# Optimization experiments

Measured on AMD Instinct MI355X. Metric: run time of the kernel, lower is better.

Reference implementation:

```python
import jax, jax.numpy as jnp
import numpy as np

B, D, N, H = 2, 512, 2048, 8
DK = D // H
EPS = 1e-5


def conv1x1(x, w, b):
    # kernel-size-1 Conv1d == channel-mixing GEMM: (o,i) x (b,i,n) -> (b,o,n)
    return jnp.einsum('oi,bin->bon', w, x) + b[None, :, None]


def setup_inputs() -> dict:
    key = jax.random.key(0)
    ks = jax.random.split(key, 20)
    s = 0.02
    return {
        'init_query': jax.random.normal(ks[0], (B, D, N), jnp.float32),
        'key_t': jax.random.normal(ks[1], (B, D, N), jnp.float32),
        'value': jax.random.normal(ks[2], (B, D, N), jnp.float32),
        'mask': jax.random.randint(ks[3], (B, 1, N, N), 0, 2, jnp.int32),
        'Wq': jax.random.normal(ks[4], (D, D), jnp.float32) * s,
        'bq': jax.random.normal(ks[5], (D,), jnp.float32) * s,
        'Wk': jax.random.normal(ks[6], (D, D), jnp.float32) * s,
        'bk': jax.random.normal(ks[7], (D,), jnp.float32) * s,
        'Wv': jax.random.normal(ks[8], (D, D), jnp.float32) * s,
        'bv': jax.random.normal(ks[9], (D,), jnp.float32) * s,
        'Wm': jax.random.normal(ks[10], (D, D), jnp.float32) * s,
        'bm': jax.random.normal(ks[11], (D,), jnp.float32) * s,
        'W1': jax.random.normal(ks[12], (2 * D, 2 * D), jnp.float32) * s,
        'b1': jax.random.normal(ks[13], (2 * D,), jnp.float32) * s,
        'gamma': jnp.ones((2 * D,), jnp.float32),
        'beta': jnp.zeros((2 * D,), jnp.float32),
        'rmean': jax.random.normal(ks[14], (2 * D,), jnp.float32) * s,
        'rvar': jnp.abs(jax.random.normal(ks[15], (2 * D,), jnp.float32)) * 0.1 + 0.5,
        'W2': jax.random.normal(ks[16], (D, 2 * D), jnp.float32) * s,
        'b2': jnp.zeros((D,), jnp.float32),  # nn.init.constant_(bias, 0.0)
    }


def reference(init_query, key_t, value, mask, Wq, bq, Wk, bk, Wv, bv, Wm, bm,
              W1, b1, gamma, beta, rmean, rvar, W2, b2):
    # projections, split channels into (d_k, n_heads) exactly like torch .view
    q = conv1x1(init_query, Wq, bq).reshape(B, DK, H, N)
    k = conv1x1(key_t, Wk, bk).reshape(B, DK, H, N)
    v = conv1x1(value, Wv, bv).reshape(B, DK, H, N)
    scores = jnp.einsum('bdhn,bdhm->bhnm', q, k) / jnp.sqrt(jnp.float32(DK))
    scores = jnp.where(mask == 0, jnp.float32(-1e9), scores)
    attn = jax.nn.softmax(scores, axis=-1)
    x = jnp.einsum('bhnm,bdhm->bdhn', attn, v).reshape(B, D, N)
    x = conv1x1(x, Wm, bm)
    x = jnp.concatenate([x, init_query], axis=1)  # (B, 2D, N)
    h = conv1x1(x, W1, b1)
    # BatchNorm1d (inference mode with running stats) + ReLU
    h = (h - rmean[None, :, None]) * (gamma / jnp.sqrt(rvar + EPS))[None, :, None] + beta[None, :, None]
    h = jax.nn.relu(h)
    return conv1x1(h, W2, b2)
```

## Files before the change

### kernel.cpp

```cpp
#include <hip/hip_runtime.h>

typedef unsigned short u16;
typedef unsigned int u32;
typedef unsigned long long u64;
typedef long long i64;
typedef __bf16 bf16x8 __attribute__((ext_vector_type(8)));
typedef u16 u16x8 __attribute__((ext_vector_type(8)));
typedef float f32x4 __attribute__((ext_vector_type(4)));
typedef float f32x16 __attribute__((ext_vector_type(16)));

#define DEV __device__ __forceinline__

constexpr int BB = 2, DD = 512, NN = 2048, HH = 8, DKc = 64, D2 = 1024;

constexpr float QSC = 0.125f * 1.44269504088896340736f;

constexpr i64 MB = 1048576;
constexpr i64 OFF_CAT = 0;
constexpr i64 OFF_XKT = 8 * MB;
constexpr i64 OFF_XVT = 12 * MB;
constexpr i64 OFF_QH  = 16 * MB;
constexpr i64 OFF_KH  = 20 * MB;
constexpr i64 OFF_VT  = 24 * MB;
constexpr i64 OFF_HT  = 28 * MB;
constexpr i64 OFF_OP  = 36 * MB;
constexpr i64 OFF_LP  = 68 * MB;
constexpr i64 OFF_WQP = 69 * MB;
constexpr i64 OFF_WKP = 69 * MB + 524288;
constexpr i64 OFF_WVP = 69 * MB + 1048576;
constexpr i64 OFF_WMT = 69 * MB + 1572864;
constexpr i64 OFF_W1A = 71 * MB;
constexpr i64 OFF_W1C = 72 * MB;
constexpr i64 OFF_W2B = 74 * MB;
constexpr i64 OFF_BQP = 75 * MB;
constexpr i64 OFF_BKP = 75 * MB + 2048;
constexpr i64 OFF_BVP = 75 * MB + 4096;
constexpr i64 OFF_BNA = 75 * MB + 8192;
constexpr i64 OFF_BNC = 75 * MB + 12288;
constexpr i64 OFF_MSK = 76 * MB;

DEV u16 f2bf(float f) {
  u32 u = __float_as_uint(f);
  u = u + 0x7FFFu + ((u >> 16) & 1u);
  return (u16)(u >> 16);
}

DEV float bf2f(u16 u) { return __uint_as_float(((u32)u) << 16); }
DEV float bf2f32(u32 u) { return __uint_as_float(u << 16); }

DEV u32 packbf(float lo, float hi) {
  return __builtin_amdgcn_perm(__float_as_uint(hi), __float_as_uint(lo), 0x07060302u);
}

DEV float fexp2(float x) {
#if __has_builtin(__builtin_amdgcn_exp2f)
  return __builtin_amdgcn_exp2f(x);
#else
  return exp2f(x);
#endif
}

DEV bf16x8 ldfrag(const u16* p) {
  bf16x8 v;
  __builtin_memcpy(&v, __builtin_assume_aligned(p, 16), 16);
  return v;
}

DEV bf16x8 ldfrag2(const u16* p0, const u16* p1) {
  bf16x8 v;
  __builtin_memcpy(&v, __builtin_assume_aligned(p0, 8), 8);
  __builtin_memcpy((char*)&v + 8, __builtin_assume_aligned(p1, 8), 8);
  return v;
}

DEV bf16x8 ones8() {
  u16x8 u = {0x3F80, 0x3F80, 0x3F80, 0x3F80, 0x3F80, 0x3F80, 0x3F80, 0x3F80};
  bf16x8 v;
  __builtin_memcpy(&v, &u, 16);
  return v;
}

DEV void gload16(const void* g, void* lds) {
  __builtin_amdgcn_global_load_lds((__attribute__((address_space(1))) void*)g,
                                   (__attribute__((address_space(3))) void*)lds, 16, 0, 0);
}

DEV f32x4 mfma16(bf16x8 a, bf16x8 b, f32x4 c) {
  return __builtin_amdgcn_mfma_f32_16x16x32_bf16(a, b, c, 0, 0, 0);
}

DEV f32x16 mfma32(bf16x8 a, bf16x8 b, f32x16 c) {
  return __builtin_amdgcn_mfma_f32_32x32x16_bf16(a, b, c, 0, 0, 0);
}

__global__ __launch_bounds__(256) void prep_all(
    const float* __restrict__ Wq, const float* __restrict__ Wk, const float* __restrict__ Wv,
    const float* __restrict__ Wm, const float* __restrict__ W1, const float* __restrict__ W2,
    const float* __restrict__ bq, const float* __restrict__ bk, const float* __restrict__ bv,
    const float* __restrict__ bm, const float* __restrict__ b1, const float* __restrict__ gamma_,
    const float* __restrict__ beta_, const float* __restrict__ rmean,
    const float* __restrict__ rvar, const int* __restrict__ mask,
    const float* __restrict__ iq, const float* __restrict__ kt, const float* __restrict__ vv,
    u16* __restrict__ wqp, u16* __restrict__ wkp, u16* __restrict__ wvp, u16* __restrict__ wmt,
    u16* __restrict__ w1a, u16* __restrict__ w1c, u16* __restrict__ w2b,
    float* __restrict__ bqp, float* __restrict__ bkp, float* __restrict__ bvp,
    float* __restrict__ bna, float* __restrict__ bnc, u32* __restrict__ mw,
    u16* __restrict__ cat, u16* __restrict__ xkt, u16* __restrict__ xvt) {
  __shared__ float tile[32][33];
  const int blk = blockIdx.x, t = threadIdx.x;
  if (blk < 768) {
    const int which = blk >> 8, lb = blk & 255;
    const float* W = which == 0 ? Wq : (which == 1 ? Wk : Wv);
    u16* dst = which == 0 ? wqp : (which == 1 ? wkp : wvp);
    for (int e = lb * 256 + t; e < 262144; e += 65536) {
      int op = e >> 9, i = e & 511;
      int dk = op & 63, h = op >> 6;
      dst[e] = f2bf(W[(dk * 8 + h) * 512 + i]);
    }
  } else if (blk < 1024) {
    const int lb = blk - 768;
    for (int e = lb * 256 + t; e < 262144; e += 65536) {
      int cp = e >> 9, o = e & 511;
      int dk = cp & 63, h = cp >> 6;
      wmt[e] = f2bf(Wm[o * 512 + dk * 8 + h]);
    }
  } else if (blk < 1280) {
    const int lb = blk - 1024;
    for (int e = lb * 256 + t; e < 524288; e += 65536) {
      int row = e >> 9, o = e & 511;
      w1a[e] = f2bf(W1[(i64)row * 1024 + o]);
    }
  } else if (blk < 1536) {
    const int lb = blk - 1280;
    for (int e = lb * 256 + t; e < 524288; e += 65536) {
      int row = e >> 9, j = e & 511;
      w1c[(i64)row * 1024 + 512 + j] = f2bf(W1[(i64)row * 1024 + 512 + j]);
    }
  } else if (blk < 1792) {
    const int lb = blk - 1536;
    for (int e = lb * 256 + t; e < 524288; e += 65536) w2b[e] = f2bf(W2[e]);
  } else if (blk < 1808) {
    __shared__ float sm[4][64];
    const int base = (blk - 1792) * 64;
    const int el = t & 63, oq = t >> 6;
    const float* wrow = W1 + (i64)(base + el) * 1024 + oq * 128;
    const float* bmq = bm + oq * 128;
    float s = 0.f;
#pragma unroll 8
    for (int j = 0; j < 128; j += 4) {
      float4 x = *(const float4*)(wrow + j);
      float4 y = *(const float4*)(bmq + j);
      s += x.x * y.x + x.y * y.y + x.z * y.z + x.w * y.w;
    }
    sm[oq][el] = s;
    __syncthreads();
    if (t < 64) {
      int e = base + t;
      float a = gamma_[e] * rsqrtf(rvar[e] + 1e-5f);
      bna[e] = a;
      bnc[e] = (b1[e] - rmean[e]) * a + beta_[e] + a * (sm[0][t] + sm[1][t] + sm[2][t] + sm[3][t]);
    }
  } else if (blk == 1808) {
    for (int e = t; e < 512; e += 256) {
      int src = (e & 63) * 8 + (e >> 6);
      bqp[e] = bq[src]; bkp[e] = bk[src]; bvp[e] = bv[src];
    }
  } else if (blk < 2833) {
    const int tid = (blk - 1809) * 256 + t;
    const i64 base = (i64)tid * 32;
    const int4* mp = (const int4*)(mask + base);
    u32 word = 0;
#pragma unroll
    for (int j = 0; j < 8; ++j) {
      int4 x = mp[j];
      u32 nib = (x.x != 0 ? 1u : 0u) | (x.y != 0 ? 2u : 0u) | (x.z != 0 ? 4u : 0u) |
                (x.w != 0 ? 8u : 0u);
      word |= nib << (j * 4);
    }
    mw[tid] = word;
  } else {
    const int idx = blk - 2833;
    const int bx = idx & 63, by = (idx >> 6) & 15, bz = idx >> 10;
    const int tensor = bz >> 1, b = bz & 1;
    const float* src = (tensor == 0 ? iq : (tensor == 1 ? kt : vv)) + (i64)b * DD * NN;
    u16* dst; i64 ldd; int coff;
    if (tensor == 0)      { dst = cat + (i64)b * NN * D2; ldd = D2; coff = DD; }
    else if (tensor == 1) { dst = xkt + (i64)b * NN * DD; ldd = DD; coff = 0; }
    else                  { dst = xvt + (i64)b * NN * DD; ldd = DD; coff = 0; }
    const int x0 = bx * 32, y0 = by * 32;
    const int col = t & 31, rg = t >> 5;
#pragma unroll
    for (int i = 0; i < 4; ++i) {
      int row = rg + i * 8;
      tile[row][col] = src[(i64)(y0 + row) * NN + x0 + col];
    }
    __syncthreads();
    const int dp = t & 15, rbase = t >> 4;
    u32* dst32 = (u32*)dst;
    const i64 ldw = ldd >> 1;
    const int cw = (coff + y0) >> 1;
#pragma unroll
    for (int i = 0; i < 2; ++i) {
      int rr = rbase + i * 16;
      dst32[(i64)(x0 + rr) * ldw + cw + dp] = packbf(tile[2 * dp][rr], tile[2 * dp + 1][rr]);
    }
  }
}

template <int AM, int AN>
DEV void gemm_core(const u16* __restrict__ A, i64 lda, const u16* __restrict__ Bp, i64 ldb,
                   int K, u16* As, u16* Bs, f32x4 (&acc)[AM][AN]) {
  constexpr int BM = AM * 32, BN = AN * 32;
  const int t = threadIdx.x, w = t >> 6, l = t & 63, quad = l >> 4, l15 = l & 15;
  const int wm = (w >> 1) * AM * 16, wn = (w & 1) * AN * 16;
  for (int kk = 0; kk < K; kk += 64) {
    __syncthreads();
#pragma unroll
    for (int j = 0; j < BM / 32; ++j) {
      int ch = j * 256 + w * 64 + l, r = ch >> 3, c = ch & 7;
      gload16(A + (i64)r * lda + kk + ((c ^ (r & 7)) << 3), As + (j * 256 + w * 64) * 8);
    }
#pragma unroll
    for (int j = 0; j < BN / 32; ++j) {
      int ch = j * 256 + w * 64 + l, r = ch >> 3, c = ch & 7;
      gload16(Bp + (i64)r * ldb + kk + ((c ^ (r & 7)) << 3), Bs + (j * 256 + w * 64) * 8);
    }
    __syncthreads();
#pragma unroll
    for (int kc = 0; kc < 2; ++kc) {
      const int sw = ((kc * 4 + quad) ^ (l15 & 7)) << 3;
      bf16x8 af[AM], bfr[AN];
#pragma unroll
      for (int i = 0; i < AM; ++i) af[i] = ldfrag(&As[(wm + i * 16 + l15) * 64 + sw]);
#pragma unroll
      for (int j = 0; j < AN; ++j) bfr[j] = ldfrag(&Bs[(wn + j * 16 + l15) * 64 + sw]);
#pragma unroll
      for (int i = 0; i < AM; ++i)
#pragma unroll
        for (int j = 0; j < AN; ++j) acc[i][j] = mfma16(af[i], bfr[j], acc[i][j]);
    }
  }
}

__global__ __launch_bounds__(256) void qkv_gemm(const u16* __restrict__ cat,
                                                const u16* __restrict__ xkt,
                                                const u16* __restrict__ xvt,
                                                const u16* __restrict__ wqp,
                                                const u16* __restrict__ wkp,
                                                const u16* __restrict__ wvp,
                                                const u16* __restrict__ w1a,
                                                const u16* __restrict__ wmt,
                                                const float* __restrict__ bqp,
                                                const float* __restrict__ bkp,
                                                const float* __restrict__ bvp,
                                                u16* __restrict__ qh, u16* __restrict__ kh,
                                                u16* __restrict__ vt, u16* __restrict__ w1c) {
  __shared__ __align__(16) u16 As[128 * 64];
  __shared__ __align__(16) u16 Bs[128 * 64];
  const int flat = blockIdx.x;
  const int t = threadIdx.x, w = t >> 6, l = t & 63, quad = l >> 4, l15 = l & 15;
  const int wm = (w >> 1) * 64, wn = (w & 1) * 64;
  int op, b = 0, mx, ny;
  if (flat < 256) {
    op = flat >> 7;
    b = (flat >> 6) & 1;
    const int r = flat & 63;
    mx = r >> 2; ny = r & 3;
  } else if (flat < 384) {
    op = 2;
    const int r = flat - 256;
    b = r >> 6;
    const int rr = r & 63;
    mx = rr >> 4; ny = rr & 15;
  } else {
    op = 3;
    const int r = flat - 384;
    mx = r >> 2; ny = r & 3;
  }
  const u16 *A, *Bp;
  i64 lda, ldb;
  if (op < 2) {
    A = (op == 0 ? cat + DD : xkt);
    lda = (op == 0 ? D2 : DD);
    A += (i64)b * NN * lda + (i64)mx * 128 * lda;
    Bp = (op == 0 ? wqp : wkp) + (i64)ny * 128 * DD;
    ldb = DD;
  } else if (op == 2) {
    A = wvp + (i64)mx * 128 * DD; lda = DD;
    Bp = xvt + (i64)b * NN * DD + (i64)ny * 128 * DD; ldb = DD;
  } else {
    A = w1a + (i64)mx * 128 * DD; lda = DD;
    Bp = wmt + (i64)ny * 128 * DD; ldb = DD;
  }
  f32x4 acc[4][4] = {};
  gemm_core<4, 4>(A, lda, Bp, ldb, DD, As, Bs, acc);

  const int rowBase = mx * 128 + wm + quad * 4;
  const int colBase = ny * 128 + wn + l15;
  if (op < 2) {
    const float* bias = (op == 0 ? bqp : bkp);
    const float sc = (op == 0 ? QSC : 1.f);
    u16* dst = (op == 0 ? qh : kh) + (i64)b * HH * NN * DKc;
#pragma unroll
    for (int j = 0; j < 4; ++j) {
      const int col = colBase + j * 16;
      const float cA = bias[col];
#pragma unroll
      for (int i = 0; i < 4; ++i)
#pragma unroll
        for (int r = 0; r < 4; ++r) {
          const int row = rowBase + i * 16 + r;
          dst[(i64)(col >> 6) * (NN * 64) + (i64)row * 64 + (col & 63)] =
              f2bf((acc[i][j][r] + cA) * sc);
        }
    }
  } else if (op == 2) {
    u16* dst = vt + (i64)b * HH * DKc * NN;
#pragma unroll
    for (int j = 0; j < 4; ++j) {
      const int col = colBase + j * 16;
#pragma unroll
      for (int i = 0; i < 4; ++i)
#pragma unroll
        for (int r = 0; r < 4; ++r) {
          const int row = rowBase + i * 16 + r;
          dst[(i64)row * NN + col] = f2bf(acc[i][j][r] + bvp[row]);
        }
    }
  } else {
#pragma unroll
    for (int j = 0; j < 4; ++j) {
      const int col = colBase + j * 16;
#pragma unroll
      for (int i = 0; i < 4; ++i)
#pragma unroll
        for (int r = 0; r < 4; ++r) {
          const int row = rowBase + i * 16 + r;
          w1c[(i64)row * D2 + col] = f2bf(acc[i][j][r]);
        }
    }
  }
}

struct GArgs {
  const u16* A; i64 lda, sAb;
  const u16* B; i64 ldb, sBb;
  void* C; i64 ldc, sCb;
  const float* p1; const float* p2;
  int K;
};

template <int MODE, int AM, int AN, int SWZ>
__global__ __launch_bounds__(256) void gemm_bt(GArgs g) {
  __shared__ __align__(16) u16 As[AM * 32 * 64];
  __shared__ __align__(16) u16 Bs[AN * 32 * 64];
  const int t = threadIdx.x, w = t >> 6, l = t & 63, quad = l >> 4, l15 = l & 15;
  const int wm = (w >> 1) * AM * 16, wn = (w & 1) * AN * 16;
  int bx = blockIdx.x, by = blockIdx.y, bz = blockIdx.z;
  if (SWZ == 1) {
    const int i = bx + (by << 3) + (bz << 8);
    const int slot = i & 7, jj = i >> 3;
    by = slot + ((jj & 3) << 3);
    const int j2 = jj >> 2;
    bx = j2 & 7;
    bz = j2 >> 3;
  }
  const u16* A = g.A + (i64)bz * g.sAb + (i64)bx * (AM * 32) * g.lda;
  const u16* Bp = g.B + (i64)bz * g.sBb + (i64)by * (AN * 32) * g.ldb;
  f32x4 acc[AM][AN] = {};
  gemm_core<AM, AN>(A, g.lda, Bp, g.ldb, g.K, As, Bs, acc);

  const int rowBase = bx * (AM * 32) + wm + quad * 4;
  const int colBase = by * (AN * 32) + wn + l15;
#pragma unroll
  for (int j = 0; j < AN; ++j) {
    const int col = colBase + j * 16;
    float cA = 0.f, cB = 0.f;
    if (MODE == 3) { cA = g.p1[col]; cB = g.p2[col]; }
#pragma unroll
    for (int i = 0; i < AM; ++i) {
#pragma unroll
      for (int r = 0; r < 4; ++r) {
        const int row = rowBase + i * 16 + r;
        float v = acc[i][j][r];
        if (MODE == 3) {
          float x = v * cA + cB;
          ((u16*)g.C + (i64)bz * g.sCb)[(i64)row * g.ldc + col] = f2bf(x > 0.f ? x : 0.f);
        } else {
          ((float*)g.C + (i64)bz * g.sCb)[(i64)row * g.ldc + col] = v + g.p1[row];
        }
      }
    }
  }
}

__global__ __launch_bounds__(512) void flash_attn(const u16* __restrict__ Qh,
                                                  const u16* __restrict__ Kh,
                                                  const u16* __restrict__ Vt,
                                                  const u64* __restrict__ MW64,
                                                  u16* __restrict__ Opart,
                                                  float* __restrict__ Lp) {
  __shared__ __align__(16) u16 Ks0[64 * 64];
  __shared__ __align__(16) u16 Ks1[64 * 64];
  __shared__ __align__(16) u16 Vs0[64 * 64];
  __shared__ __align__(16) u16 Vs1[64 * 64];
  const int t = threadIdx.x, w = t >> 6, l = t & 63, l31 = l & 31, lh = l >> 5;
  const int flat = blockIdx.x;
  const int h = flat & 7;
  const int j = flat >> 3;
  const int nt = j & 7, zz = j >> 3;
  const int sp = zz & 3, b = zz >> 2;
  const int n = nt * 256 + w * 32 + l31;
  const u16* Qb = Qh + ((i64)(b * HH + h) * NN + nt * 256 + w * 32) * 64;
  const u16* Kb = Kh + (i64)(b * HH + h) * NN * 64;
  const u16* Vb = Vt + (i64)(b * HH + h) * 64 * NN;
  const u64* mwp = MW64 + (i64)(b * NN + n) * 32;
  const bf16x8 ONE = ones8();
  bf16x8 qf[4];
#pragma unroll
  for (int kc = 0; kc < 4; ++kc)
    __builtin_memcpy(&qf[kc], Qb + (i64)l31 * 64 + kc * 16 + lh * 8, 16);

  f32x16 oacc0 = {}, oacc1 = {}, lacc = {};
  const int mt0 = sp * 8;

  auto stage = [&](u16* Kd, u16* Vd, int mt) {
    const int r = t >> 3, c = t & 7;
    gload16(Kb + (i64)(mt * 64 + r) * 64 + ((c ^ (r & 7)) << 3), Kd + t * 8);
    gload16(Vb + (i64)r * NN + mt * 64 + ((c ^ (r & 7)) << 3), Vd + t * 8);
  };
  auto compute = [&](const u16* Kc, const u16* Vc, int mt) {
    f32x16 s0 = {}, s1 = {};
#pragma unroll
    for (int kc = 0; kc < 4; ++kc) {
      const int sw = l31 & 7;
      bf16x8 k0 = ldfrag(&Kc[l31 * 64 + (((kc * 2 + lh) ^ sw) << 3)]);
      bf16x8 k1 = ldfrag(&Kc[(32 + l31) * 64 + (((kc * 2 + lh) ^ sw) << 3)]);
      s0 = mfma32(k0, qf[kc], s0);
      s1 = mfma32(k1, qf[kc], s1);
    }
    const u64 mrow = mwp[mt];
    u32 pw[16];
#pragma unroll
    for (int k = 0; k < 8; ++k) {
      const int kvb = ((2 * k) & 3) + 8 * ((2 * k) >> 2) + 4 * lh;
      u64 sh = mrow >> kvb;
      u32 mA = (((u32)sh & 1u) | (((u32)sh & 2u) << 15)) * 0xFFFFu;
      u32 shh = (u32)(sh >> 32);
      u32 mB = ((shh & 1u) | ((shh & 2u) << 15)) * 0xFFFFu;
      pw[k] = packbf(fexp2(s0[2 * k]), fexp2(s0[2 * k + 1])) & mA;
      pw[8 + k] = packbf(fexp2(s1[2 * k]), fexp2(s1[2 * k + 1])) & mB;
    }
    bf16x8 pf[4];
#pragma unroll
    for (int c = 0; c < 4; ++c) __builtin_memcpy(&pf[c], &pw[c * 4], 16);
#pragma unroll
    for (int c = 0; c < 4; ++c) lacc = mfma32(ONE, pf[c], lacc);
#pragma unroll
    for (int c = 0; c < 4; ++c) {
      const int sw0 = l31 & 7;
      const u16* r0 = &Vc[l31 * 64];
      const u16* r1 = &Vc[(32 + l31) * 64];
      bf16x8 v0 = ldfrag2(r0 + (((2 * c) ^ sw0) << 3) + lh * 4,
                          r0 + (((2 * c + 1) ^ sw0) << 3) + lh * 4);
      bf16x8 v1 = ldfrag2(r1 + (((2 * c) ^ sw0) << 3) + lh * 4,
                          r1 + (((2 * c + 1) ^ sw0) << 3) + lh * 4);
      oacc0 = mfma32(v0, pf[c], oacc0);
      oacc1 = mfma32(v1, pf[c], oacc1);
    }
  };

  stage(Ks0, Vs0, mt0);
#pragma unroll
  for (int i = 0; i < 8; i += 2) {
    __syncthreads();
    stage(Ks1, Vs1, mt0 + i + 1);
    compute(Ks0, Vs0, mt0 + i);
    __syncthreads();
    if (i + 2 < 8) stage(Ks0, Vs0, mt0 + i + 2);
    compute(Ks1, Vs1, mt0 + i + 1);
  }
  u16* OpT = Opart + ((i64)((sp * BB + b) * HH + h) * 64) * NN;
#pragma unroll
  for (int r = 0; r < 16; ++r) {
    const int d0 = (r & 3) + 8 * (r >> 2) + 4 * lh;
    OpT[(i64)d0 * NN + n] = f2bf(oacc0[r]);
    OpT[(i64)(d0 + 32) * NN + n] = f2bf(oacc1[r]);
  }
  if (lh == 0) Lp[((i64)(sp * BB + b) * HH + h) * NN + n] = lacc[0];
}

__global__ __launch_bounds__(256) void combine(const u16* __restrict__ Opart,
                                               const float* __restrict__ Lp,
                                               u16* __restrict__ cat) {
  __shared__ float lt[128 * 65];
  const int t = threadIdx.x;
  const int nt = blockIdx.x, bh = blockIdx.y;
  const int b = bh >> 3, h = bh & 7;
  const int n0 = nt * 128;
  const i64 sstride = (i64)BB * HH * 64 * NN;
  const u16* Ob = Opart + ((i64)(b * HH + h) * 64) * NN;
#pragma unroll
  for (int i = 0; i < 16; ++i) {
    const int idx = i * 256 + t;
    const int d = idx >> 6, np = idx & 63;
    float sa = 0.f, sb = 0.f;
#pragma unroll
    for (int s = 0; s < 4; ++s) {
      u32 v;
      __builtin_memcpy(&v, Ob + s * sstride + (i64)d * NN + n0 + 2 * np, 4);
      sa += bf2f32(v & 0xFFFFu);
      sb += bf2f32(v >> 16);
    }
    lt[(2 * np) * 65 + d] = sa;
    lt[(2 * np + 1) * 65 + d] = sb;
  }
  __syncthreads();
  u32* catw = (u32*)cat;
#pragma unroll
  for (int i = 0; i < 16; ++i) {
    const int idx = i * 256 + t;
    const int nn = idx >> 5, dp = idx & 31;
    float lsum = 0.f;
#pragma unroll
    for (int s = 0; s < 4; ++s) lsum += Lp[((i64)(s * BB + b) * HH + h) * NN + n0 + nn];
    const float rl = __builtin_amdgcn_rcpf(lsum);
    u32 pv = packbf(lt[nn * 65 + 2 * dp] * rl, lt[nn * 65 + 2 * dp + 1] * rl);
    catw[((i64)b * NN + n0 + nn) * (D2 / 2) + h * 32 + dp] = pv;
  }
}

extern "C" void kernel_launch(void* const* d_in, const int* in_sizes, int n_in,
                              void* d_out, int out_size, void* d_ws, size_t ws_size,
                              hipStream_t stream) {
  (void)in_sizes; (void)n_in; (void)out_size; (void)ws_size;
  const float* iq    = (const float*)d_in[0];
  const float* kt    = (const float*)d_in[1];
  const float* vv    = (const float*)d_in[2];
  const int*   mask  = (const int*)d_in[3];
  const float* Wq    = (const float*)d_in[4];
  const float* bq    = (const float*)d_in[5];
  const float* Wk    = (const float*)d_in[6];
  const float* bk    = (const float*)d_in[7];
  const float* Wv    = (const float*)d_in[8];
  const float* bv    = (const float*)d_in[9];
  const float* Wm    = (const float*)d_in[10];
  const float* bm    = (const float*)d_in[11];
  const float* W1    = (const float*)d_in[12];
  const float* b1    = (const float*)d_in[13];
  const float* gamma_= (const float*)d_in[14];
  const float* beta_ = (const float*)d_in[15];
  const float* rmean = (const float*)d_in[16];
  const float* rvar  = (const float*)d_in[17];
  const float* W2    = (const float*)d_in[18];
  const float* b2    = (const float*)d_in[19];

  char* ws = (char*)d_ws;
  u16* cat = (u16*)(ws + OFF_CAT);
  u16* xkt = (u16*)(ws + OFF_XKT);
  u16* xvt = (u16*)(ws + OFF_XVT);
  u16* qh  = (u16*)(ws + OFF_QH);
  u16* kh  = (u16*)(ws + OFF_KH);
  u16* vt  = (u16*)(ws + OFF_VT);
  u16* ht  = (u16*)(ws + OFF_HT);
  u16* opart = (u16*)(ws + OFF_OP);
  float* lp  = (float*)(ws + OFF_LP);
  u16* wqp = (u16*)(ws + OFF_WQP);
  u16* wkp = (u16*)(ws + OFF_WKP);
  u16* wvp = (u16*)(ws + OFF_WVP);
  u16* wmt = (u16*)(ws + OFF_WMT);
  u16* w1a = (u16*)(ws + OFF_W1A);
  u16* w1c = (u16*)(ws + OFF_W1C);
  u16* w2b = (u16*)(ws + OFF_W2B);
  float* bqp = (float*)(ws + OFF_BQP);
  float* bkp = (float*)(ws + OFF_BKP);
  float* bvp = (float*)(ws + OFF_BVP);
  float* bna = (float*)(ws + OFF_BNA);
  float* bnc = (float*)(ws + OFF_BNC);
  u32* mw = (u32*)(ws + OFF_MSK);

  prep_all<<<8977, 256, 0, stream>>>(Wq, Wk, Wv, Wm, W1, W2, bq, bk, bv, bm, b1, gamma_, beta_,
                                     rmean, rvar, mask, iq, kt, vv, wqp, wkp, wvp, wmt, w1a, w1c,
                                     w2b, bqp, bkp, bvp, bna, bnc, mw, cat, xkt, xvt);
  qkv_gemm<<<416, 256, 0, stream>>>(cat, xkt, xvt, wqp, wkp, wvp, w1a, wmt,
                                    bqp, bkp, bvp, qh, kh, vt, w1c);
  flash_attn<<<512, 512, 0, stream>>>(qh, kh, vt, (const u64*)mw, opart, lp);
  combine<<<dim3(16, 16), 256, 0, stream>>>(opart, lp, cat);
  GArgs wa{cat, D2, 0, w1c, D2, 0, ht, D2, 0, bna, bnc, D2};
  gemm_bt<3, 4, 2, 0><<<dim3(32, 16, 1), 256, 0, stream>>>(wa);
  GArgs w2a{w2b, D2, 0, ht, D2, (i64)NN * D2, d_out, NN, (i64)DD * NN, b2, nullptr, D2};
  gemm_bt<4, 2, 2, 1><<<dim3(8, 32, 2), 256, 0, stream>>>(w2a);
}
```

Before: 216.5 us.

## Double-buffer shared-memory tiles in GEMM core to overlap loads with MFMA

Turns the GEMM main loop into a two-stage pipeline. The next K-slice is loaded asynchronously into a second LDS buffer while the current slice feeds MFMA, with one barrier per iteration instead of two. Shared-memory footprint doubles in both qkv_gemm and gemm_bt, which may lower occupancy. Because of the full vmcnt(0) wait at the end of each iteration, the overlap is limited to the MFMA work within that iteration.

```diff
diff --git a/kernel.cpp b/kernel.cpp
--- a/kernel.cpp
+++ b/kernel.cpp
@@ -213,32 +213,43 @@
   constexpr int BM = AM * 32, BN = AN * 32;
   const int t = threadIdx.x, w = t >> 6, l = t & 63, quad = l >> 4, l15 = l & 15;
   const int wm = (w >> 1) * AM * 16, wn = (w & 1) * AN * 16;
-  for (int kk = 0; kk < K; kk += 64) {
-    __syncthreads();
+  auto stage = [&](int kk, int buf) {
+    u16* Ad = As + buf * (BM * 64);
+    u16* Bd = Bs + buf * (BN * 64);
 #pragma unroll
     for (int j = 0; j < BM / 32; ++j) {
       int ch = j * 256 + w * 64 + l, r = ch >> 3, c = ch & 7;
-      gload16(A + (i64)r * lda + kk + ((c ^ (r & 7)) << 3), As + (j * 256 + w * 64) * 8);
+      gload16(A + (i64)r * lda + kk + ((c ^ (r & 7)) << 3), Ad + (j * 256 + w * 64) * 8);
     }
 #pragma unroll
     for (int j = 0; j < BN / 32; ++j) {
       int ch = j * 256 + w * 64 + l, r = ch >> 3, c = ch & 7;
-      gload16(Bp + (i64)r * ldb + kk + ((c ^ (r & 7)) << 3), Bs + (j * 256 + w * 64) * 8);
-    }
-    __syncthreads();
+      gload16(Bp + (i64)r * ldb + kk + ((c ^ (r & 7)) << 3), Bd + (j * 256 + w * 64) * 8);
+    }
+  };
+  const int nst = K >> 6;
+  stage(0, 0);
+  asm volatile("s_waitcnt vmcnt(0)" ::: "memory");
+  __builtin_amdgcn_s_barrier();
+  for (int s = 0; s < nst; ++s) {
+    if (s + 1 < nst) stage((s + 1) << 6, (s + 1) & 1);
+    const u16* Ac = As + (s & 1) * (BM * 64);
+    const u16* Bc = Bs + (s & 1) * (BN * 64);
 #pragma unroll
     for (int kc = 0; kc < 2; ++kc) {
       const int sw = ((kc * 4 + quad) ^ (l15 & 7)) << 3;
       bf16x8 af[AM], bfr[AN];
 #pragma unroll
-      for (int i = 0; i < AM; ++i) af[i] = ldfrag(&As[(wm + i * 16 + l15) * 64 + sw]);
-#pragma unroll
-      for (int j = 0; j < AN; ++j) bfr[j] = ldfrag(&Bs[(wn + j * 16 + l15) * 64 + sw]);
+      for (int i = 0; i < AM; ++i) af[i] = ldfrag(&Ac[(wm + i * 16 + l15) * 64 + sw]);
+#pragma unroll
+      for (int j = 0; j < AN; ++j) bfr[j] = ldfrag(&Bc[(wn + j * 16 + l15) * 64 + sw]);
 #pragma unroll
       for (int i = 0; i < AM; ++i)
 #pragma unroll
         for (int j = 0; j < AN; ++j) acc[i][j] = mfma16(af[i], bfr[j], acc[i][j]);
     }
+    asm volatile("s_waitcnt vmcnt(0) lgkmcnt(0)" ::: "memory");
+    __builtin_amdgcn_s_barrier();
   }
 }
 
@@ -255,8 +266,8 @@
                                                 const float* __restrict__ bvp,
                                                 u16* __restrict__ qh, u16* __restrict__ kh,
                                                 u16* __restrict__ vt, u16* __restrict__ w1c) {
-  __shared__ __align__(16) u16 As[128 * 64];
-  __shared__ __align__(16) u16 Bs[128 * 64];
+  __shared__ __align__(16) u16 As[2 * 128 * 64];
+  __shared__ __align__(16) u16 Bs[2 * 128 * 64];
   const int flat = blockIdx.x;
   const int t = threadIdx.x, w = t >> 6, l = t & 63, quad = l >> 4, l15 = l & 15;
   const int wm = (w >> 1) * 64, wn = (w & 1) * 64;
@@ -352,8 +363,8 @@
 
 template <int MODE, int AM, int AN, int SWZ>
 __global__ __launch_bounds__(256) void gemm_bt(GArgs g) {
-  __shared__ __align__(16) u16 As[AM * 32 * 64];
-  __shared__ __align__(16) u16 Bs[AN * 32 * 64];
+  __shared__ __align__(16) u16 As[2 * AM * 32 * 64];
+  __shared__ __align__(16) u16 Bs[2 * AN * 32 * 64];
   const int t = threadIdx.x, w = t >> 6, l = t & 63, quad = l >> 4, l15 = l & 15;
   const int wm = (w >> 1) * AM * 16, wn = (w & 1) * AN * 16;
   int bx = blockIdx.x, by = blockIdx.y, bz = blockIdx.z;
```

Result: no change. 215.9 us (-0.3%).
